# Performance work log

Hardware: AMD Instinct MI355X
Metric: run time of the kernel (lower is better)

## Reference

```python
import jax, jax.numpy as jnp
import numpy as np

B, H, W, DIN = 512, 14, 14, 512
EDIM, K = 64, 256
GRID = 2  # code grid -> code_seq_len = 4


def setup_inputs() -> dict:
    key = jax.random.key(0)
    ks = jax.random.split(key, 12)
    def lin(k, fin, fout):
        return jax.random.normal(k, (fin, fout), jnp.float32) / np.sqrt(fin).astype(np.float32)
    return {
        "features_t0": jax.random.normal(ks[0], (B, H, W, DIN), jnp.float32),
        "features_t1": jax.random.normal(ks[1], (B, H, W, DIN), jnp.float32),
        "enc_w1": lin(ks[2], DIN, 2 * EDIM), "enc_b1": jnp.zeros((2 * EDIM,), jnp.float32),
        "enc_w2": lin(ks[3], 2 * EDIM, EDIM), "enc_b2": jnp.zeros((EDIM,), jnp.float32),
        "dec_w1": lin(ks[4], EDIM, 2 * EDIM), "dec_b1": jnp.zeros((2 * EDIM,), jnp.float32),
        "dec_w2": lin(ks[5], 2 * EDIM, DIN), "dec_b2": jnp.zeros((DIN,), jnp.float32),
        "codebook": jax.random.normal(ks[6], (K, EDIM), jnp.float32),
    }


def reference(features_t0, features_t1, enc_w1, enc_b1, enc_w2, enc_b2,
              dec_w1, dec_b1, dec_w2, dec_b2, codebook):
    # eval-mode forward (no EMA update / data init)
    delta = features_t1 - features_t0                       # [B,H,W,DIN]
    h = jax.nn.gelu(delta @ enc_w1 + enc_b1, approximate=False)
    e = h @ enc_w2 + enc_b2                                 # [B,H,W,EDIM]
    # AdaptiveAvgPool2d((2,2)) on 14x14 == exact 7x7 block mean
    bh, bw = H // GRID, W // GRID
    pooled = e.reshape(B, GRID, bh, GRID, bw, EDIM).mean(axis=(2, 4))  # [B,2,2,EDIM]
    enc = pooled.reshape(B, GRID * GRID, EDIM)              # [B,4,EDIM]

    flat = enc.reshape(-1, EDIM)                            # [B*4, EDIM]
    d2 = ((flat ** 2).sum(-1, keepdims=True)
          - 2.0 * flat @ codebook.T
          + (codebook ** 2).sum(-1))                        # [N,K]
    idx = jnp.argmin(d2, axis=1)                            # [N]
    quantized = codebook[idx]                               # [N,EDIM]

    commitment_loss = jnp.mean((jax.lax.stop_gradient(quantized) - flat) ** 2)
    q_st = flat + jax.lax.stop_gradient(quantized - flat)   # straight-through

    n_tok = flat.shape[0]
    avg_probs = jnp.zeros((K,), flat.dtype).at[idx].add(1.0) / n_tok
    perplexity = jnp.exp(-jnp.sum(avg_probs * jnp.log(avg_probs + 1e-10)))

    q = q_st.reshape(B, GRID * GRID, EDIM)
    hd = jax.nn.gelu(q @ dec_w1 + dec_b1, approximate=False)
    dec = hd @ dec_w2 + dec_b2                              # [B,4,DIN]
    sp = dec.reshape(B, GRID, GRID, DIN).transpose(0, 3, 1, 2)  # [B,DIN,2,2]
    # bilinear, align_corners=False (half-pixel centers, matches jax.image.resize)
    up = jax.image.resize(sp, (B, DIN, H, W), method="bilinear")
    decoded = up.transpose(0, 2, 3, 1)                      # [B,H,W,DIN]

    indices = idx.reshape(B, GRID * GRID)
    return decoded, perplexity, commitment_loss, indices
```

## Files before the change

### kernel.cpp

```cpp
#include <hip/hip_runtime.h>
#include <math.h>

#define N_TOKENS   2048
#define DECODED_SZ 51380224

typedef __attribute__((ext_vector_type(8)))  short bf16x8;
typedef __attribute__((ext_vector_type(16))) float f32x16;

__device__ __forceinline__ float gelu_exact(float x) {
    return 0.5f * x * (1.0f + erff(x * 0.70710678118654752440f));
}

__device__ __forceinline__ unsigned int f2bf(float x) {
    unsigned int u = __float_as_uint(x);
    return (u + 0x7fffu + ((u >> 16) & 1u)) >> 16;
}
__device__ __forceinline__ float bf2f(unsigned int b) {
    return __uint_as_float(b << 16);
}

__global__ __launch_bounds__(256) void k0_prep_w1(
    const float* __restrict__ w1,
    unsigned short* __restrict__ bth, unsigned short* __restrict__ btl)
{
    const int i  = blockIdx.x * 256 + threadIdx.x;
    const int n  = i >> 6;
    const int kg = i & 63;
    const int k0i = kg * 8;

    unsigned int h[8], lo[8];
#pragma unroll
    for (int j = 0; j < 8; ++j) {
        float v = w1[(k0i + j) * 128 + n];
        h[j]  = f2bf(v);
        lo[j] = f2bf(v - bf2f(h[j]));
    }
    const int idx = (k0i >> 5) * 4096 + n * 32 + (k0i & 31);
    uint4 hv, lv;
    hv.x = h[0]  | (h[1] << 16);  hv.y = h[2]  | (h[3] << 16);
    hv.z = h[4]  | (h[5] << 16);  hv.w = h[6]  | (h[7] << 16);
    lv.x = lo[0] | (lo[1] << 16); lv.y = lo[2] | (lo[3] << 16);
    lv.z = lo[4] | (lo[5] << 16); lv.w = lo[6] | (lo[7] << 16);
    *reinterpret_cast<uint4*>(bth + idx) = hv;
    *reinterpret_cast<uint4*>(btl + idx) = lv;
}

__global__ __launch_bounds__(256, 2) void k1_enc_pool(
    const float* __restrict__ t0, const float* __restrict__ t1,
    const unsigned short* __restrict__ bth, const unsigned short* __restrict__ btl,
    const float* __restrict__ b1,
    float* __restrict__ pooled)
{
    __shared__ unsigned short sAh[256 * 40];
    __shared__ unsigned short sAl[256 * 40];
    __shared__ unsigned short sBh[128 * 40];
    __shared__ unsigned short sBl[128 * 40];
    __shared__ float sR[2 * 4 * 128];

    const int t = threadIdx.x;
    const int b = blockIdx.x;
    const int l     = t & 63;
    const int w     = t >> 6;
    const int wm    = w >> 1;
    const int wn    = w & 1;
    const int lan31 = l & 31;
    const int h     = l >> 5;

    const float4* __restrict__ t0v = reinterpret_cast<const float4*>(t0);
    const float4* __restrict__ t1v = reinterpret_cast<const float4*>(t1);

    f32x16 acc[4][2] = {};

    for (int kc = 0; kc < 16; ++kc) {
        __syncthreads();
        for (int i = t; i < 196 * 8; i += 256) {
            const int m = i >> 3, j = i & 7;
            const int g4 = (b * 196 + m) * 128 + kc * 8 + j;
            const float4 a = t1v[g4];
            const float4 c = t0v[g4];
            const float dx = a.x - c.x, dy = a.y - c.y, dz = a.z - c.z, dw = a.w - c.w;
            const unsigned int h0 = f2bf(dx), h1 = f2bf(dy), h2 = f2bf(dz), h3 = f2bf(dw);
            const unsigned int l0 = f2bf(dx - bf2f(h0)), l1 = f2bf(dy - bf2f(h1));
            const unsigned int l2 = f2bf(dz - bf2f(h2)), l3 = f2bf(dw - bf2f(h3));
            uint2 hv, lv;
            hv.x = h0 | (h1 << 16); hv.y = h2 | (h3 << 16);
            lv.x = l0 | (l1 << 16); lv.y = l2 | (l3 << 16);
            *reinterpret_cast<uint2*>(&sAh[m * 40 + j * 4]) = hv;
            *reinterpret_cast<uint2*>(&sAl[m * 40 + j * 4]) = lv;
        }
        for (int i = t; i < 1024; i += 256) {
            const int sel = i >> 9;
            const int i2 = i & 511;
            const int col = i2 >> 2, j8 = i2 & 3;
            const uint4 v = *reinterpret_cast<const uint4*>(
                (sel ? btl : bth) + kc * 4096 + col * 32 + j8 * 8);
            *reinterpret_cast<uint4*>(&(sel ? sBl : sBh)[col * 40 + j8 * 8]) = v;
        }
        __syncthreads();

#pragma unroll
        for (int ks = 0; ks < 2; ++ks) {
            const int koff = ks * 16 + h * 8;
            bf16x8 ah[4], al[4], bhf[2], blf[2];
#pragma unroll
            for (int mi = 0; mi < 4; ++mi) {
                const int row = (wm * 4 + mi) * 32 + lan31;
                ah[mi] = *reinterpret_cast<const bf16x8*>(&sAh[row * 40 + koff]);
                al[mi] = *reinterpret_cast<const bf16x8*>(&sAl[row * 40 + koff]);
            }
#pragma unroll
            for (int ni = 0; ni < 2; ++ni) {
                const int col = (wn * 2 + ni) * 32 + lan31;
                bhf[ni] = *reinterpret_cast<const bf16x8*>(&sBh[col * 40 + koff]);
                blf[ni] = *reinterpret_cast<const bf16x8*>(&sBl[col * 40 + koff]);
            }
#pragma unroll
            for (int mi = 0; mi < 4; ++mi) {
#pragma unroll
                for (int ni = 0; ni < 2; ++ni) {
                    acc[mi][ni] = __builtin_amdgcn_mfma_f32_32x32x16_bf16(
                        ah[mi], bhf[ni], acc[mi][ni], 0, 0, 0);
                    acc[mi][ni] = __builtin_amdgcn_mfma_f32_32x32x16_bf16(
                        ah[mi], blf[ni], acc[mi][ni], 0, 0, 0);
                    acc[mi][ni] = __builtin_amdgcn_mfma_f32_32x32x16_bf16(
                        al[mi], bhf[ni], acc[mi][ni], 0, 0, 0);
                }
            }
        }
    }

    float tokacc[2][4] = {};
#pragma unroll
    for (int ni = 0; ni < 2; ++ni) {
        const int col = (wn * 2 + ni) * 32 + lan31;
        const float bias = b1[col];
#pragma unroll
        for (int mi = 0; mi < 4; ++mi) {
#pragma unroll
            for (int reg = 0; reg < 16; ++reg) {
                const int row = (wm * 4 + mi) * 32 + (reg & 3) + 8 * (reg >> 2) + 4 * h;
                if (row < 196) {
                    const float v = gelu_exact(acc[mi][ni][reg] + bias);
                    const int py = row / 14, px = row % 14;
                    const int tok = ((py >= 7) ? 2 : 0) + ((px >= 7) ? 1 : 0);
                    tokacc[ni][tok] += v;
                }
            }
        }
    }
#pragma unroll
    for (int ni = 0; ni < 2; ++ni)
#pragma unroll
        for (int tok = 0; tok < 4; ++tok)
            tokacc[ni][tok] += __shfl_xor(tokacc[ni][tok], 32);
    if (h == 0) {
#pragma unroll
        for (int ni = 0; ni < 2; ++ni)
#pragma unroll
            for (int tok = 0; tok < 4; ++tok)
                sR[(wm * 4 + tok) * 128 + wn * 64 + ni * 32 + lan31] = tokacc[ni][tok];
    }
    __syncthreads();
    for (int i = t; i < 512; i += 256) {
        const int tok = i >> 7, col = i & 127;
        pooled[(b * 4 + tok) * 128 + col] =
            (sR[tok * 128 + col] + sR[(4 + tok) * 128 + col]) * (1.0f / 49.0f);
    }
}

__global__ __launch_bounds__(256, 2) void k2_mid(
    const float* __restrict__ pooled,
    const float* __restrict__ w2,  const float* __restrict__ b2,
    const float* __restrict__ cb,
    const float* __restrict__ dw1, const float* __restrict__ db1,
    const float* __restrict__ dw2, const float* __restrict__ db2,
    float* __restrict__ dec, float* __restrict__ hist, float* __restrict__ commit,
    float* __restrict__ out_idx)
{
    __shared__ float sCB[256 * 66];
    __shared__ float ph[4 * 128];
    __shared__ float es[4 * 64];
    __shared__ float hd[4 * 128];
    __shared__ float rd[256];
    __shared__ int   ri[256];
    __shared__ int   idxs[4];
    __shared__ float dms[4];

    const int t   = threadIdx.x;
    const int tk0 = blockIdx.x * 4;

    if (t < 128)
        reinterpret_cast<float4*>(ph)[t] =
            reinterpret_cast<const float4*>(pooled + tk0 * 128)[t];
    for (int i = t; i < 16384; i += 256) {
        int row = i >> 6, k = i & 63;
        sCB[row * 66 + k] = cb[i];
    }
    __syncthreads();

    {
        const int j = t & 63, tok = t >> 6;
        float a = b2[j];
        const float* phr = ph + tok * 128;
#pragma unroll 8
        for (int k = 0; k < 128; ++k)
            a = fmaf(phr[k], w2[k * 64 + j], a);
        es[tok * 64 + j] = a;
    }
    __syncthreads();

    {
        const int tok = t >> 6, c8 = t & 63;
        float2 ev[32];
#pragma unroll
        for (int k = 0; k < 32; ++k)
            ev[k] = *reinterpret_cast<const float2*>(es + tok * 64 + 2 * k);
        float dmin = 3.4e38f; int imin = 0;
#pragma unroll
        for (int cc = 0; cc < 4; ++cc) {
            const int c = c8 + cc * 64;
            const float* cr = sCB + c * 66;
            float d = 0.f;
#pragma unroll
            for (int k = 0; k < 32; ++k) {
                float2 c2 = *reinterpret_cast<const float2*>(cr + 2 * k);
                float d0 = ev[k].x - c2.x;
                float d1 = ev[k].y - c2.y;
                d = fmaf(d0, d0, d);
                d = fmaf(d1, d1, d);
            }
            if (d < dmin || (d == dmin && c < imin)) { dmin = d; imin = c; }
        }
        rd[t] = dmin; ri[t] = imin;
    }
    __syncthreads();
    for (int s = 32; s > 0; s >>= 1) {
        if ((t & 63) < s) {
            float dn = rd[t + s]; int in = ri[t + s];
            if (dn < rd[t] || (dn == rd[t] && in < ri[t])) { rd[t] = dn; ri[t] = in; }
        }
        __syncthreads();
    }
    if ((t & 63) == 0) {
        const int tok = t >> 6;
        idxs[tok] = ri[t];
        dms[tok]  = rd[t];
        out_idx[tk0 + tok] = (float)ri[t];
        atomicAdd(&hist[ri[t]], 1.0f);
    }
    __syncthreads();
    if (t == 0) {
        float s = dms[0] + dms[1] + dms[2] + dms[3];
        atomicAdd(commit, s);
    }

    {
        const int j = t & 127, half = t >> 7;
        const float bj = db1[j];
        float a0 = bj, a1 = bj;
        const float* q0 = sCB + idxs[half * 2 + 0] * 66;
        const float* q1 = sCB + idxs[half * 2 + 1] * 66;
#pragma unroll 4
        for (int k = 0; k < 64; ++k) {
            const float wv = dw1[k * 128 + j];
            a0 = fmaf(q0[k], wv, a0);
            a1 = fmaf(q1[k], wv, a1);
        }
        hd[(half * 2 + 0) * 128 + j] = gelu_exact(a0);
        hd[(half * 2 + 1) * 128 + j] = gelu_exact(a1);
    }
    __syncthreads();

    {
        float a0[4], a1[4];
        const float bb0 = db2[t], bb1 = db2[t + 256];
#pragma unroll
        for (int q = 0; q < 4; ++q) { a0[q] = bb0; a1[q] = bb1; }
#pragma unroll 2
        for (int j = 0; j < 128; ++j) {
            const float w0 = dw2[j * 512 + t];
            const float w1v = dw2[j * 512 + 256 + t];
#pragma unroll
            for (int q = 0; q < 4; ++q) {
                const float h = hd[q * 128 + j];
                a0[q] = fmaf(h, w0, a0[q]);
                a1[q] = fmaf(h, w1v, a1[q]);
            }
        }
#pragma unroll
        for (int q = 0; q < 4; ++q) {
            dec[(tk0 + q) * 512 + t]       = a0[q];
            dec[(tk0 + q) * 512 + 256 + t] = a1[q];
        }
    }
}

__global__ __launch_bounds__(256) void k2b_final(
    const float* __restrict__ hist, const float* __restrict__ commit,
    float* __restrict__ out2)
{
    __shared__ float red[256];
    const int t = threadIdx.x;
    float p = hist[t] * (1.0f / 2048.0f);
    red[t] = p * logf(p + 1e-10f);
    __syncthreads();
    for (int s = 128; s > 0; s >>= 1) {
        if (t < s) red[t] += red[t + s];
        __syncthreads();
    }
    if (t == 0) {
        out2[0] = expf(-red[0]);
        out2[1] = commit[0] * (1.0f / 131072.0f);
    }
}

__global__ __launch_bounds__(256, 4) void k3_upsample(
    const float* __restrict__ dec, float* __restrict__ out)
{
    __shared__ float  sdec[4 * 512];
    __shared__ float4 wts[196];
    __shared__ int4   offs[196];
    const int b = blockIdx.x, t = threadIdx.x;

    for (int i = t; i < 512; i += 256)
        reinterpret_cast<float4*>(sdec)[i] =
            reinterpret_cast<const float4*>(dec + b * 2048)[i];
    if (t < 196) {
        const int y = t / 14, x = t % 14;
        const float sy = (y + 0.5f) * (1.0f / 7.0f) - 0.5f;
        const float sx = (x + 0.5f) * (1.0f / 7.0f) - 0.5f;
        const int iy = (int)floorf(sy), ix = (int)floorf(sx);
        const float fy = sy - (float)iy, fx = sx - (float)ix;
        const int y0 = min(max(iy, 0), 1), y1 = min(max(iy + 1, 0), 1);
        const int x0 = min(max(ix, 0), 1), x1 = min(max(ix + 1, 0), 1);
        float4 w;
        w.x = (1.f - fy) * (1.f - fx); w.y = (1.f - fy) * fx;
        w.z = fy * (1.f - fx);         w.w = fy * fx;
        wts[t] = w;
        int4 o;
        o.x = (y0 * 2 + x0) * 128; o.y = (y0 * 2 + x1) * 128;
        o.z = (y1 * 2 + x0) * 128; o.w = (y1 * 2 + x1) * 128;
        offs[t] = o;
    }
    __syncthreads();

    const float4* s4 = reinterpret_cast<const float4*>(sdec);
    float4* o4 = reinterpret_cast<float4*>(out) + b * 25088;
    const int c4 = t & 127, ph2 = t >> 7;

#pragma unroll 2
    for (int it = 0; it < 98; ++it) {
        const int pos = ph2 + it * 2;
        const float4 w = wts[pos];
        const int4   o = offs[pos];
        const float4 v00 = s4[o.x + c4];
        const float4 v01 = s4[o.y + c4];
        const float4 v10 = s4[o.z + c4];
        const float4 v11 = s4[o.w + c4];
        float4 r;
        r.x = w.x * v00.x + w.y * v01.x + w.z * v10.x + w.w * v11.x;
        r.y = w.x * v00.y + w.y * v01.y + w.z * v10.y + w.w * v11.y;
        r.z = w.x * v00.z + w.y * v01.z + w.z * v10.z + w.w * v11.z;
        r.w = w.x * v00.w + w.y * v01.w + w.z * v10.w + w.w * v11.w;
        o4[pos * 128 + c4] = r;
    }
}

extern "C" void kernel_launch(void* const* d_in, const int* in_sizes, int n_in,
                              void* d_out, int out_size, void* d_ws, size_t ws_size,
                              hipStream_t stream)
{
    const float* t0  = (const float*)d_in[0];
    const float* t1  = (const float*)d_in[1];
    const float* w1  = (const float*)d_in[2];
    const float* b1  = (const float*)d_in[3];
    const float* w2  = (const float*)d_in[4];
    const float* b2  = (const float*)d_in[5];
    const float* dw1 = (const float*)d_in[6];
    const float* db1 = (const float*)d_in[7];
    const float* dw2 = (const float*)d_in[8];
    const float* db2 = (const float*)d_in[9];
    const float* cb  = (const float*)d_in[10];

    float* out = (float*)d_out;
    float* ws  = (float*)d_ws;

    float* pooled = ws;
    float* dec    = ws + 262144;
    float* hist   = ws + 1310720;
    float* commit = ws + 1310976;

    unsigned short* bth = (unsigned short*)(ws + 262144);
    unsigned short* btl = (unsigned short*)(ws + 262144 + 32768);

    hipMemsetAsync(hist, 0, 257 * sizeof(float), stream);

    k0_prep_w1<<<32, 256, 0, stream>>>(w1, bth, btl);
    k1_enc_pool<<<512, 256, 0, stream>>>(t0, t1, bth, btl, b1, pooled);
    k2_mid<<<512, 256, 0, stream>>>(pooled, w2, b2, cb, dw1, db1, dw2, db2,
                                    dec, hist, commit, out + DECODED_SZ + 2);
    k2b_final<<<1, 256, 0, stream>>>(hist, commit, out + DECODED_SZ);
    k3_upsample<<<512, 256, 0, stream>>>(dec, out);
}
```

Baseline: 630.0 us.

## Load MFMA operands directly from global memory, bypassing LDS staging

The encoder GEMM kernel no longer stages the delta tile and the split weights through shared memory. Each lane now loads its own A-fragment rows from t0/t1, computes the difference, and splits it into bf16 hi/lo using the packed v_cvt_pk_bf16_f32 instruction. B fragments are read straight from global memory. Fully padded M tiles are skipped, and the two __syncthreads per k-chunk are gone. The cost is uncoalesced, strided per-lane global loads (each row touches 32 bytes) and extra global traffic for B, which is reloaded by every wave.

```diff
diff --git a/kernel.cpp b/kernel.cpp
--- a/kernel.cpp
+++ b/kernel.cpp
@@ -6,6 +6,7 @@
 
 typedef __attribute__((ext_vector_type(8)))  short bf16x8;
 typedef __attribute__((ext_vector_type(16))) float f32x16;
+typedef __attribute__((ext_vector_type(4)))  unsigned int u32x4;
 
 __device__ __forceinline__ float gelu_exact(float x) {
     return 0.5f * x * (1.0f + erff(x * 0.70710678118654752440f));
@@ -18,6 +19,21 @@
 __device__ __forceinline__ float bf2f(unsigned int b) {
     return __uint_as_float(b << 16);
 }
+
+__device__ __forceinline__ unsigned int cvt_pk_bf16(float a, float b) {
+    unsigned int p;
+    asm("v_cvt_pk_bf16_f32 %0, %1, %2" : "=v"(p) : "v"(a), "v"(b));
+    return p;
+}
+__device__ __forceinline__ void split_pair(float a, float b,
+                                           unsigned int& hi, unsigned int& lo) {
+    hi = cvt_pk_bf16(a, b);
+    const float ra = a - __uint_as_float(hi << 16);
+    const float rb = b - __uint_as_float(hi & 0xffff0000u);
+    lo = cvt_pk_bf16(ra, rb);
+}
+
+union UF { u32x4 u; bf16x8 v; };
 
 __global__ __launch_bounds__(256) void k0_prep_w1(
     const float* __restrict__ w1,
@@ -51,10 +67,6 @@
     const float* __restrict__ b1,
     float* __restrict__ pooled)
 {
-    __shared__ unsigned short sAh[256 * 40];
-    __shared__ unsigned short sAl[256 * 40];
-    __shared__ unsigned short sBh[128 * 40];
-    __shared__ unsigned short sBl[128 * 40];
     __shared__ float sR[2 * 4 * 128];
 
     const int t = threadIdx.x;
@@ -71,59 +83,71 @@
 
     f32x16 acc[4][2] = {};
 
+    int gbase[4];
+    int valid[4];
+#pragma unroll
+    for (int mi = 0; mi < 4; ++mi) {
+        const int row = (wm * 4 + mi) * 32 + lan31;
+        valid[mi] = (row < 196);
+        gbase[mi] = (b * 196 + (row < 196 ? row : 0)) * 128 + h * 2;
+    }
+    int boff[2][2];
+#pragma unroll
+    for (int ni = 0; ni < 2; ++ni) {
+        const int col = (wn * 2 + ni) * 32 + lan31;
+#pragma unroll
+        for (int ks = 0; ks < 2; ++ks)
+            boff[ni][ks] = col * 32 + ks * 16 + h * 8;
+    }
+
+#pragma unroll 1
     for (int kc = 0; kc < 16; ++kc) {
-        __syncthreads();
-        for (int i = t; i < 196 * 8; i += 256) {
-            const int m = i >> 3, j = i & 7;
-            const int g4 = (b * 196 + m) * 128 + kc * 8 + j;
-            const float4 a = t1v[g4];
-            const float4 c = t0v[g4];
-            const float dx = a.x - c.x, dy = a.y - c.y, dz = a.z - c.z, dw = a.w - c.w;
-            const unsigned int h0 = f2bf(dx), h1 = f2bf(dy), h2 = f2bf(dz), h3 = f2bf(dw);
-            const unsigned int l0 = f2bf(dx - bf2f(h0)), l1 = f2bf(dy - bf2f(h1));
-            const unsigned int l2 = f2bf(dz - bf2f(h2)), l3 = f2bf(dw - bf2f(h3));
-            uint2 hv, lv;
-            hv.x = h0 | (h1 << 16); hv.y = h2 | (h3 << 16);
-            lv.x = l0 | (l1 << 16); lv.y = l2 | (l3 << 16);
-            *reinterpret_cast<uint2*>(&sAh[m * 40 + j * 4]) = hv;
-            *reinterpret_cast<uint2*>(&sAl[m * 40 + j * 4]) = lv;
-        }
-        for (int i = t; i < 1024; i += 256) {
-            const int sel = i >> 9;
-            const int i2 = i & 511;
-            const int col = i2 >> 2, j8 = i2 & 3;
-            const uint4 v = *reinterpret_cast<const uint4*>(
-                (sel ? btl : bth) + kc * 4096 + col * 32 + j8 * 8);
-            *reinterpret_cast<uint4*>(&(sel ? sBl : sBh)[col * 40 + j8 * 8]) = v;
-        }
-        __syncthreads();
-
-#pragma unroll
-        for (int ks = 0; ks < 2; ++ks) {
-            const int koff = ks * 16 + h * 8;
-            bf16x8 ah[4], al[4], bhf[2], blf[2];
-#pragma unroll
-            for (int mi = 0; mi < 4; ++mi) {
-                const int row = (wm * 4 + mi) * 32 + lan31;
-                ah[mi] = *reinterpret_cast<const bf16x8*>(&sAh[row * 40 + koff]);
-                al[mi] = *reinterpret_cast<const bf16x8*>(&sAl[row * 40 + koff]);
+        bf16x8 bh[2][2], bl[2][2];
+#pragma unroll
+        for (int ni = 0; ni < 2; ++ni)
+#pragma unroll
+            for (int ks = 0; ks < 2; ++ks) {
+                bh[ni][ks] = *reinterpret_cast<const bf16x8*>(
+                    bth + kc * 4096 + boff[ni][ks]);
+                bl[ni][ks] = *reinterpret_cast<const bf16x8*>(
+                    btl + kc * 4096 + boff[ni][ks]);
             }
-#pragma unroll
-            for (int ni = 0; ni < 2; ++ni) {
-                const int col = (wn * 2 + ni) * 32 + lan31;
-                bhf[ni] = *reinterpret_cast<const bf16x8*>(&sBh[col * 40 + koff]);
-                blf[ni] = *reinterpret_cast<const bf16x8*>(&sBl[col * 40 + koff]);
-            }
-#pragma unroll
-            for (int mi = 0; mi < 4; ++mi) {
-#pragma unroll
-                for (int ni = 0; ni < 2; ++ni) {
-                    acc[mi][ni] = __builtin_amdgcn_mfma_f32_32x32x16_bf16(
-                        ah[mi], bhf[ni], acc[mi][ni], 0, 0, 0);
-                    acc[mi][ni] = __builtin_amdgcn_mfma_f32_32x32x16_bf16(
-                        ah[mi], blf[ni], acc[mi][ni], 0, 0, 0);
-                    acc[mi][ni] = __builtin_amdgcn_mfma_f32_32x32x16_bf16(
-                        al[mi], bhf[ni], acc[mi][ni], 0, 0, 0);
+
+#pragma unroll
+        for (int mi = 0; mi < 4; ++mi) {
+            const int mt = wm * 4 + mi;
+            if (mt < 7) {
+#pragma unroll
+                for (int ks = 0; ks < 2; ++ks) {
+                    float d0, d1, d2, d3, d4, d5, d6, d7;
+                    if (valid[mi]) {
+                        const int g = gbase[mi] + kc * 8 + ks * 4;
+                        const float4 x0 = t1v[g],     y0 = t0v[g];
+                        const float4 x1 = t1v[g + 1], y1 = t0v[g + 1];
+                        d0 = x0.x - y0.x; d1 = x0.y - y0.y;
+                        d2 = x0.z - y0.z; d3 = x0.w - y0.w;
+                        d4 = x1.x - y1.x; d5 = x1.y - y1.y;
+                        d6 = x1.z - y1.z; d7 = x1.w - y1.w;
+                    } else {
+                        d0 = d1 = d2 = d3 = d4 = d5 = d6 = d7 = 0.0f;
+                    }
+                    UF ah, al;
+                    {
+                        unsigned int hw, lw;
+                        split_pair(d0, d1, hw, lw); ah.u[0] = hw; al.u[0] = lw;
+                        split_pair(d2, d3, hw, lw); ah.u[1] = hw; al.u[1] = lw;
+                        split_pair(d4, d5, hw, lw); ah.u[2] = hw; al.u[2] = lw;
+                        split_pair(d6, d7, hw, lw); ah.u[3] = hw; al.u[3] = lw;
+                    }
+#pragma unroll
+                    for (int ni = 0; ni < 2; ++ni) {
+                        acc[mi][ni] = __builtin_amdgcn_mfma_f32_32x32x16_bf16(
+                            ah.v, bh[ni][ks], acc[mi][ni], 0, 0, 0);
+                        acc[mi][ni] = __builtin_amdgcn_mfma_f32_32x32x16_bf16(
+                            ah.v, bl[ni][ks], acc[mi][ni], 0, 0, 0);
+                        acc[mi][ni] = __builtin_amdgcn_mfma_f32_32x32x16_bf16(
+                            al.v, bh[ni][ks], acc[mi][ni], 0, 0, 0);
+                    }
                 }
             }
         }
```

New measurement: 632.7 us. No clear change (+0.4%).
